# Kernel optimization log

Hardware: AMD Instinct MI355X
Metric: run time of the kernel (lower is better)

The kernel has to match this reference:

```python
import jax, jax.numpy as jnp
import numpy as np

N = 100000
E = 1600000
DIM = 64
HEADS = 8
HEAD_DIM = DIM // HEADS
LN_EPS = 1e-5
NORM_EPS = 1e-12


def setup_inputs() -> dict:
    key = jax.random.key(0)
    ks = jax.random.split(key, 5)
    x = jax.random.normal(ks[0], (N, DIM), dtype=jnp.float32)
    edge_index = jax.random.randint(ks[1], (2, E), 0, N, dtype=jnp.int32)
    W_w = jax.random.normal(ks[2], (DIM, DIM), dtype=jnp.float32) * (1.0 / np.sqrt(DIM))
    W_b = jax.random.normal(ks[3], (DIM,), dtype=jnp.float32) * 0.01
    a = jax.random.normal(ks[4], (HEADS, 2 * HEAD_DIM), dtype=jnp.float32) * 0.1
    ln_scale = jnp.ones((DIM,), dtype=jnp.float32)
    ln_bias = jnp.zeros((DIM,), dtype=jnp.float32)
    return {"x": x, "edge_index": edge_index, "W_w": W_w, "W_b": W_b,
            "a": a, "ln_scale": ln_scale, "ln_bias": ln_bias}


def reference(x, edge_index, W_w, W_b, a, ln_scale, ln_bias):
    n = x.shape[0]
    # Linear (dropout = identity in eval), reshape to heads
    h = (x @ W_w.T + W_b).reshape(n, HEADS, HEAD_DIM)          # [N,H,D]
    src, dst = edge_index[0], edge_index[1]
    hs = h[src]                                                 # [E,H,D]
    hd = h[dst]                                                 # [E,H,D]
    a_src, a_dst = a[:, :HEAD_DIM], a[:, HEAD_DIM:]             # [H,D] each
    # (a * cat(hs, hd)).sum(-1) split over the two halves
    alpha = jnp.einsum('ehd,hd->eh', hs, a_src) + jnp.einsum('ehd,hd->eh', hd, a_dst)
    alpha = jnp.where(alpha >= 0, alpha, 0.2 * alpha)           # LeakyReLU(0.2)
    alpha = jax.nn.softmax(alpha, axis=1)                       # NOTE: over heads, as in source
    msg = alpha[..., None] * hd                                 # [E,H,D]
    out = jax.ops.segment_sum(msg, src, num_segments=n)         # scatter-add to src nodes
    out = out.reshape(n, DIM)
    # residual + LayerNorm
    y = out + x
    mu = jnp.mean(y, axis=-1, keepdims=True)
    var = jnp.mean((y - mu) ** 2, axis=-1, keepdims=True)
    y = (y - mu) * jax.lax.rsqrt(var + LN_EPS) * ln_scale + ln_bias
    # F.normalize(p=2, dim=-1)
    norm = jnp.sqrt(jnp.sum(y * y, axis=-1, keepdims=True))
    return y / jnp.maximum(norm, NORM_EPS)
```

## Files before the change

### kernel.cpp

```cpp
#include <hip/hip_runtime.h>
#include <hip/hip_fp16.h>
#include <math.h>

#define N_NODES 100000
#define N_EDGES 1600000
#define LN_EPS 1e-5f
#define NORM_EPS 1e-12f
#define ROWS_PER_BLOCK 32
#define GEMM_BLOCKS (N_NODES / ROWS_PER_BLOCK)
#define WSTRIDE 66
#define REC_BYTES 32
#define WB 64
#define NBKT ((N_NODES + WB - 1) / WB)
#define BIN_TILE 8192
#define BIN_BLOCKS ((N_EDGES + BIN_TILE - 1) / BIN_TILE)

__global__ __launch_bounds__(256) void k_gemm(
    const float* __restrict__ x, const float* __restrict__ W,
    const float* __restrict__ b, const float* __restrict__ a,
    __half* __restrict__ h16,
    float* __restrict__ s_src, float* __restrict__ s_dst)
{
    __shared__ float WL[64 * WSTRIDE];
    __shared__ float xs[ROWS_PER_BLOCK * 64];
    const int tid  = threadIdx.x;
    const int lane = tid & 63;
    const int wv   = tid >> 6;

    for (int idx = tid * 4; idx < 64 * 64; idx += 256 * 4) {
        const float4 w = *(const float4*)(W + idx);
        const int c = idx >> 6, k = idx & 63;
        WL[c * WSTRIDE + k + 0] = w.x;
        WL[c * WSTRIDE + k + 1] = w.y;
        WL[c * WSTRIDE + k + 2] = w.z;
        WL[c * WSTRIDE + k + 3] = w.w;
    }
    const int row0 = blockIdx.x * ROWS_PER_BLOCK;
    for (int idx = tid * 4; idx < ROWS_PER_BLOCK * 64; idx += 256 * 4)
        *(float4*)(xs + idx) = *(const float4*)(x + (size_t)row0 * 64 + idx);
    __syncthreads();

    const float bias = b[lane];
    float acc[8];
    #pragma unroll
    for (int r = 0; r < 8; ++r) acc[r] = bias;

    const int rbase = wv * 8;
    const float* wrow = WL + lane * WSTRIDE;
    const float* xrow = xs + rbase * 64;
    #pragma unroll 1
    for (int kk = 0; kk < 64; kk += 4) {
        const float2 w01 = *(const float2*)(wrow + kk);
        const float2 w23 = *(const float2*)(wrow + kk + 2);
        #pragma unroll
        for (int r = 0; r < 8; ++r) {
            const float4 xq = *(const float4*)(xrow + r * 64 + kk);
            acc[r] += xq.x * w01.x + xq.y * w01.y + xq.z * w23.x + xq.w * w23.y;
        }
    }

    const float asrc = a[(lane >> 3) * 16 + (lane & 7)];
    const float adst = a[(lane >> 3) * 16 + 8 + (lane & 7)];
    #pragma unroll
    for (int r = 0; r < 8; ++r) {
        const int row = row0 + rbase + r;
        const float v = acc[r];
        h16[(size_t)row * 64 + lane] = __float2half_rn(v);
        float p = v * asrc, q = v * adst;
        p += __shfl_xor(p, 1);  q += __shfl_xor(q, 1);
        p += __shfl_xor(p, 2);  q += __shfl_xor(q, 2);
        p += __shfl_xor(p, 4);  q += __shfl_xor(q, 4);
        if ((lane & 7) == 0) {
            s_src[row * 8 + (lane >> 3)] = p;
            s_dst[row * 8 + (lane >> 3)] = q;
        }
    }
}

__global__ __launch_bounds__(1024) void k_hist(
    const int* __restrict__ ei, int* __restrict__ bhist)
{
    __shared__ int hist[NBKT];
    const int tid = threadIdx.x;
    for (int b = tid; b < NBKT; b += 1024) hist[b] = 0;
    __syncthreads();
    const int e0 = blockIdx.x * BIN_TILE;
    #pragma unroll
    for (int j = 0; j < 8; ++j) {
        const int e = e0 + j * 1024 + tid;
        if (e < N_EDGES) atomicAdd(&hist[ei[e] >> 6], 1);
    }
    __syncthreads();
    for (int b = tid; b < NBKT; b += 1024)
        if (hist[b]) atomicAdd(&bhist[b], hist[b]);
}

__global__ __launch_bounds__(1024) void k_bscan(
    const int* __restrict__ bhist, int* __restrict__ bucket_base,
    int* __restrict__ gbin)
{
    __shared__ int wsum[16];
    const int tid = threadIdx.x, lane = tid & 63, wv = tid >> 6;

    int v = (tid < NBKT) ? bhist[tid] : 0;
    int sc = v;
    #pragma unroll
    for (int off = 1; off < 64; off <<= 1) {
        int t = __shfl_up(sc, off);
        if (lane >= off) sc += t;
    }
    if (lane == 63) wsum[wv] = sc;
    __syncthreads();
    if (tid < 16) {
        int ws = wsum[tid];
        #pragma unroll
        for (int off = 1; off < 16; off <<= 1) {
            int t = __shfl_up(ws, off);
            if (tid >= off) ws += t;
        }
        wsum[tid] = ws;
    }
    __syncthreads();
    const int pref0 = wv ? wsum[wv - 1] : 0;
    const int ex0 = pref0 + sc - v;
    if (tid < NBKT) { bucket_base[tid] = ex0; gbin[tid] = ex0; }
    const int T1 = wsum[15];
    __syncthreads();

    const int i2 = 1024 + tid;
    int v2 = (i2 < NBKT) ? bhist[i2] : 0;
    int sc2 = v2;
    #pragma unroll
    for (int off = 1; off < 64; off <<= 1) {
        int t = __shfl_up(sc2, off);
        if (lane >= off) sc2 += t;
    }
    if (lane == 63) wsum[wv] = sc2;
    __syncthreads();
    if (tid < 16) {
        int ws = wsum[tid];
        #pragma unroll
        for (int off = 1; off < 16; off <<= 1) {
            int t = __shfl_up(ws, off);
            if (tid >= off) ws += t;
        }
        wsum[tid] = ws;
    }
    __syncthreads();
    const int pref1 = wv ? wsum[wv - 1] : 0;
    const int ex1 = T1 + pref1 + sc2 - v2;
    if (i2 < NBKT) { bucket_base[i2] = ex1; gbin[i2] = ex1; }
    if (tid == 0) bucket_base[NBKT] = N_EDGES;
}

__global__ __launch_bounds__(1024) void k_bin(
    const int* __restrict__ ei, int* __restrict__ gbin,
    int2* __restrict__ staged)
{
    __shared__ int hist[NBKT];
    __shared__ int base[NBKT];
    const int tid = threadIdx.x;
    for (int b = tid; b < NBKT; b += 1024) hist[b] = 0;
    __syncthreads();

    int s[8], d[8], r[8];
    const int e0 = blockIdx.x * BIN_TILE;
    #pragma unroll
    for (int j = 0; j < 8; ++j) {
        const int e = e0 + j * 1024 + tid;
        if (e < N_EDGES) {
            s[j] = ei[e];
            d[j] = ei[N_EDGES + e];
            r[j] = atomicAdd(&hist[s[j] >> 6], 1);
        }
    }
    __syncthreads();
    for (int b = tid; b < NBKT; b += 1024)
        if (hist[b]) base[b] = atomicAdd(&gbin[b], hist[b]);
    __syncthreads();
    #pragma unroll
    for (int j = 0; j < 8; ++j) {
        const int e = e0 + j * 1024 + tid;
        if (e < N_EDGES)
            staged[(size_t)base[s[j] >> 6] + r[j]] = make_int2(s[j], d[j]);
    }
}

__global__ __launch_bounds__(1024) void k_place(
    const int* __restrict__ bucket_base, const int2* __restrict__ staged,
    const float* __restrict__ s_src, const float* __restrict__ s_dst,
    int* __restrict__ row_ptr, char* __restrict__ rec)
{
    __shared__ int cnt[WB];
    __shared__ int cur[WB];
    const int g   = blockIdx.x;
    const int n0  = g * WB;
    const int tid = threadIdx.x;
    if (tid < WB) cnt[tid] = 0;
    __syncthreads();
    const int beg = bucket_base[g];
    const int end = bucket_base[g + 1];

    for (int j = beg + tid; j < end; j += 1024)
        atomicAdd(&cnt[staged[j].x - n0], 1);
    __syncthreads();
    if (tid < WB) {
        const int c = cnt[tid];
        int sc = c;
        #pragma unroll
        for (int off = 1; off < 64; off <<= 1) {
            int t = __shfl_up(sc, off);
            if (tid >= off) sc += t;
        }
        const int rp = beg + sc - c;
        cur[tid] = rp;
        if (n0 + tid < N_NODES) row_ptr[n0 + tid] = rp;
    }
    if (g == NBKT - 1 && tid == 0) row_ptr[N_NODES] = N_EDGES;
    __syncthreads();

    for (int j = beg + tid; j < end; j += 1024) {
        const int2 sd = staged[j];
        const int src = sd.x, dst = sd.y;

        const float4 a0 = *(const float4*)(s_src + (size_t)src * 8);
        const float4 a1 = *(const float4*)(s_src + (size_t)src * 8 + 4);
        const float4 b0 = *(const float4*)(s_dst + (size_t)dst * 8);
        const float4 b1 = *(const float4*)(s_dst + (size_t)dst * 8 + 4);
        float sc[8] = {a0.x + b0.x, a0.y + b0.y, a0.z + b0.z, a0.w + b0.w,
                       a1.x + b1.x, a1.y + b1.y, a1.z + b1.z, a1.w + b1.w};
        float m = -1e30f;
        #pragma unroll
        for (int h = 0; h < 8; ++h) {
            sc[h] = (sc[h] >= 0.f) ? sc[h] : 0.2f * sc[h];
            m = fmaxf(m, sc[h]);
        }
        float sum = 0.f;
        #pragma unroll
        for (int h = 0; h < 8; ++h) { sc[h] = __expf(sc[h] - m); sum += sc[h]; }
        const float inv = 1.f / sum;
        unsigned int q[4];
        #pragma unroll
        for (int jj = 0; jj < 4; ++jj) {
            const unsigned short lo = __half_as_ushort(__float2half_rn(sc[2*jj]   * inv));
            const unsigned short hi = __half_as_ushort(__float2half_rn(sc[2*jj+1] * inv));
            q[jj] = (unsigned int)lo | ((unsigned int)hi << 16);
        }

        const int slot = atomicAdd(&cur[src - n0], 1);
        char* rcd = rec + (size_t)slot * REC_BYTES;
        *(uint4*)rcd        = make_uint4(q[0], q[1], q[2], q[3]);
        *(uint4*)(rcd + 16) = make_uint4((unsigned)dst, 0u, 0u, 0u);
    }
}

__global__ __launch_bounds__(256) void k_gather(
    const int* __restrict__ row_ptr, const char* __restrict__ rec,
    const __half* __restrict__ h16,
    const float* __restrict__ x, const float* __restrict__ ln_scale,
    const float* __restrict__ ln_bias, float* __restrict__ out)
{
    const int i = blockIdx.x * 4 + (threadIdx.x >> 6);
    if (i >= N_NODES) return;
    const int lane = threadIdx.x & 63;
    const int head = lane >> 3;

    const int beg = row_ptr[i];
    const int end = row_ptr[i + 1];
    const float xres = x[(size_t)i * 64 + lane];

    float acc = 0.f;
    int e = beg;
    for (; e + 3 < end; e += 4) {
        const char* r0 = rec + (size_t)(e + 0) * REC_BYTES;
        const char* r1 = rec + (size_t)(e + 1) * REC_BYTES;
        const char* r2 = rec + (size_t)(e + 2) * REC_BYTES;
        const char* r3 = rec + (size_t)(e + 3) * REC_BYTES;
        const int d0 = *(const int*)(r0 + 16);
        const int d1 = *(const int*)(r1 + 16);
        const int d2 = *(const int*)(r2 + 16);
        const int d3 = *(const int*)(r3 + 16);
        const float al0 = __half2float(*(const __half*)(r0 + (head << 1)));
        const float al1 = __half2float(*(const __half*)(r1 + (head << 1)));
        const float al2 = __half2float(*(const __half*)(r2 + (head << 1)));
        const float al3 = __half2float(*(const __half*)(r3 + (head << 1)));
        const float h0 = __half2float(h16[(size_t)d0 * 64 + lane]);
        const float h1 = __half2float(h16[(size_t)d1 * 64 + lane]);
        const float h2 = __half2float(h16[(size_t)d2 * 64 + lane]);
        const float h3 = __half2float(h16[(size_t)d3 * 64 + lane]);
        acc += al0 * h0 + al1 * h1 + al2 * h2 + al3 * h3;
    }
    for (; e < end; ++e) {
        const char* r = rec + (size_t)e * REC_BYTES;
        acc += __half2float(*(const __half*)(r + (head << 1))) *
               __half2float(h16[(size_t)(*(const int*)(r + 16)) * 64 + lane]);
    }

    float v = acc + xres;
    float s = v;
    #pragma unroll
    for (int off = 1; off < 64; off <<= 1) s += __shfl_xor(s, off);
    const float mu = s * (1.f / 64.f);
    const float d = v - mu;
    float vs = d * d;
    #pragma unroll
    for (int off = 1; off < 64; off <<= 1) vs += __shfl_xor(vs, off);
    const float var = vs * (1.f / 64.f);
    float y = d * rsqrtf(var + LN_EPS) * ln_scale[lane] + ln_bias[lane];
    float ss = y * y;
    #pragma unroll
    for (int off = 1; off < 64; off <<= 1) ss += __shfl_xor(ss, off);
    const float norm = sqrtf(ss);
    out[(size_t)i * 64 + lane] = y / fmaxf(norm, NORM_EPS);
}

extern "C" void kernel_launch(void* const* d_in, const int* in_sizes, int n_in,
                              void* d_out, int out_size, void* d_ws, size_t ws_size,
                              hipStream_t stream)
{
    const float* x        = (const float*)d_in[0];
    const int*   ei       = (const int*)d_in[1];
    const float* W        = (const float*)d_in[2];
    const float* b        = (const float*)d_in[3];
    const float* a        = (const float*)d_in[4];
    const float* ln_scale = (const float*)d_in[5];
    const float* ln_bias  = (const float*)d_in[6];
    float* out = (float*)d_out;

    char* ws = (char*)d_ws;
    size_t off = 0;
    auto alloc = [&](size_t bytes) {
        void* p = ws + off;
        off = (off + bytes + 255) & ~(size_t)255;
        return p;
    };
    __half* h16       = (__half*)alloc((size_t)N_NODES * 64 * 2);
    float* s_src      = (float*) alloc((size_t)N_NODES * 8 * 4);
    float* s_dst      = (float*) alloc((size_t)N_NODES * 8 * 4);
    int*   bhist      = (int*)   alloc((size_t)NBKT * 4);
    int*   bucket_base= (int*)   alloc((size_t)(NBKT + 1) * 4);
    int*   gbin       = (int*)   alloc((size_t)NBKT * 4);
    int*   row_ptr    = (int*)   alloc((size_t)(N_NODES + 1) * 4);
    int2*  staged     = (int2*)  alloc((size_t)N_EDGES * 8);
    char*  rec        = (char*)  alloc((size_t)N_EDGES * REC_BYTES);

    hipMemsetAsync(bhist, 0, (size_t)NBKT * 4, stream);

    k_hist  <<<BIN_BLOCKS, 1024, 0, stream>>>(ei, bhist);
    k_bscan <<<1, 1024, 0, stream>>>(bhist, bucket_base, gbin);
    k_gemm  <<<GEMM_BLOCKS, 256, 0, stream>>>(x, W, b, a, h16, s_src, s_dst);
    k_bin   <<<BIN_BLOCKS, 1024, 0, stream>>>(ei, gbin, staged);
    k_place <<<NBKT, 1024, 0, stream>>>(bucket_base, staged, s_src, s_dst,
                                        row_ptr, rec);
    k_gather<<<(N_NODES + 3) / 4, 256, 0, stream>>>(row_ptr, rec,
                                                    h16, x,
                                                    ln_scale, ln_bias, out);
}
```

Before: 254.1 us.

## Fuse edge placement and gather into per-bucket shared-memory scatter-add with LayerNorm

Removes the per-node CSR build (row_ptr, 32-byte edge records) and the separate gather kernel. Each 64-node bucket block now computes attention weights for chunks of its edges into LDS, then scatter-adds alpha*h[dst] into a 64x64 shared accumulator with LDS atomics, and finishes with residual, LayerNorm and L2 normalize in the same kernel. Staged edges are packed into one 32-bit word (local src in 6 bits, dst in the rest), halving staging traffic. The trade-offs are LDS atomic contention, serialized per-wave loops over 64 edges each, and only ~1563 blocks of 1024 threads for the whole gather.

```diff
diff --git a/kernel.cpp b/kernel.cpp
--- a/kernel.cpp
+++ b/kernel.cpp
@@ -9,11 +9,11 @@
 #define ROWS_PER_BLOCK 32
 #define GEMM_BLOCKS (N_NODES / ROWS_PER_BLOCK)
 #define WSTRIDE 66
-#define REC_BYTES 32
 #define WB 64
 #define NBKT ((N_NODES + WB - 1) / WB)
 #define BIN_TILE 8192
 #define BIN_BLOCKS ((N_EDGES + BIN_TILE - 1) / BIN_TILE)
+#define QCHUNK 1024
 
 __global__ __launch_bounds__(256) void k_gemm(
     const float* __restrict__ x, const float* __restrict__ W,
@@ -155,7 +155,7 @@
 
 __global__ __launch_bounds__(1024) void k_bin(
     const int* __restrict__ ei, int* __restrict__ gbin,
-    int2* __restrict__ staged)
+    unsigned int* __restrict__ staged)
 {
     __shared__ int hist[NBKT];
     __shared__ int base[NBKT];
@@ -182,136 +182,102 @@
     for (int j = 0; j < 8; ++j) {
         const int e = e0 + j * 1024 + tid;
         if (e < N_EDGES)
-            staged[(size_t)base[s[j] >> 6] + r[j]] = make_int2(s[j], d[j]);
+            staged[(size_t)base[s[j] >> 6] + r[j]] =
+                (unsigned int)((s[j] & 63) | (d[j] << 6));
     }
 }
 
 __global__ __launch_bounds__(1024) void k_place(
-    const int* __restrict__ bucket_base, const int2* __restrict__ staged,
+    const int* __restrict__ bucket_base, const unsigned int* __restrict__ staged,
     const float* __restrict__ s_src, const float* __restrict__ s_dst,
-    int* __restrict__ row_ptr, char* __restrict__ rec)
-{
-    __shared__ int cnt[WB];
-    __shared__ int cur[WB];
-    const int g   = blockIdx.x;
-    const int n0  = g * WB;
-    const int tid = threadIdx.x;
-    if (tid < WB) cnt[tid] = 0;
-    __syncthreads();
+    const __half* __restrict__ h16, const float* __restrict__ x,
+    const float* __restrict__ ln_scale, const float* __restrict__ ln_bias,
+    float* __restrict__ out)
+{
+    __shared__ float accs[WB * 64];
+    __shared__ uint4 qa[QCHUNK];
+    __shared__ unsigned int qm[QCHUNK];
+    const int g    = blockIdx.x;
+    const int n0   = g * WB;
+    const int tid  = threadIdx.x;
+    const int lane = tid & 63;
+    const int wv   = tid >> 6;
+
+    #pragma unroll
+    for (int k = tid; k < WB * 64; k += 1024) accs[k] = 0.f;
     const int beg = bucket_base[g];
     const int end = bucket_base[g + 1];
-
-    for (int j = beg + tid; j < end; j += 1024)
-        atomicAdd(&cnt[staged[j].x - n0], 1);
-    __syncthreads();
-    if (tid < WB) {
-        const int c = cnt[tid];
-        int sc = c;
-        #pragma unroll
-        for (int off = 1; off < 64; off <<= 1) {
-            int t = __shfl_up(sc, off);
-            if (tid >= off) sc += t;
-        }
-        const int rp = beg + sc - c;
-        cur[tid] = rp;
-        if (n0 + tid < N_NODES) row_ptr[n0 + tid] = rp;
-    }
-    if (g == NBKT - 1 && tid == 0) row_ptr[N_NODES] = N_EDGES;
-    __syncthreads();
-
-    for (int j = beg + tid; j < end; j += 1024) {
-        const int2 sd = staged[j];
-        const int src = sd.x, dst = sd.y;
-
-        const float4 a0 = *(const float4*)(s_src + (size_t)src * 8);
-        const float4 a1 = *(const float4*)(s_src + (size_t)src * 8 + 4);
-        const float4 b0 = *(const float4*)(s_dst + (size_t)dst * 8);
-        const float4 b1 = *(const float4*)(s_dst + (size_t)dst * 8 + 4);
-        float sc[8] = {a0.x + b0.x, a0.y + b0.y, a0.z + b0.z, a0.w + b0.w,
-                       a1.x + b1.x, a1.y + b1.y, a1.z + b1.z, a1.w + b1.w};
-        float m = -1e30f;
-        #pragma unroll
-        for (int h = 0; h < 8; ++h) {
-            sc[h] = (sc[h] >= 0.f) ? sc[h] : 0.2f * sc[h];
-            m = fmaxf(m, sc[h]);
-        }
-        float sum = 0.f;
-        #pragma unroll
-        for (int h = 0; h < 8; ++h) { sc[h] = __expf(sc[h] - m); sum += sc[h]; }
-        const float inv = 1.f / sum;
-        unsigned int q[4];
-        #pragma unroll
-        for (int jj = 0; jj < 4; ++jj) {
-            const unsigned short lo = __half_as_ushort(__float2half_rn(sc[2*jj]   * inv));
-            const unsigned short hi = __half_as_ushort(__float2half_rn(sc[2*jj+1] * inv));
-            q[jj] = (unsigned int)lo | ((unsigned int)hi << 16);
-        }
-
-        const int slot = atomicAdd(&cur[src - n0], 1);
-        char* rcd = rec + (size_t)slot * REC_BYTES;
-        *(uint4*)rcd        = make_uint4(q[0], q[1], q[2], q[3]);
-        *(uint4*)(rcd + 16) = make_uint4((unsigned)dst, 0u, 0u, 0u);
-    }
-}
-
-__global__ __launch_bounds__(256) void k_gather(
-    const int* __restrict__ row_ptr, const char* __restrict__ rec,
-    const __half* __restrict__ h16,
-    const float* __restrict__ x, const float* __restrict__ ln_scale,
-    const float* __restrict__ ln_bias, float* __restrict__ out)
-{
-    const int i = blockIdx.x * 4 + (threadIdx.x >> 6);
-    if (i >= N_NODES) return;
-    const int lane = threadIdx.x & 63;
-    const int head = lane >> 3;
-
-    const int beg = row_ptr[i];
-    const int end = row_ptr[i + 1];
-    const float xres = x[(size_t)i * 64 + lane];
-
-    float acc = 0.f;
-    int e = beg;
-    for (; e + 3 < end; e += 4) {
-        const char* r0 = rec + (size_t)(e + 0) * REC_BYTES;
-        const char* r1 = rec + (size_t)(e + 1) * REC_BYTES;
-        const char* r2 = rec + (size_t)(e + 2) * REC_BYTES;
-        const char* r3 = rec + (size_t)(e + 3) * REC_BYTES;
-        const int d0 = *(const int*)(r0 + 16);
-        const int d1 = *(const int*)(r1 + 16);
-        const int d2 = *(const int*)(r2 + 16);
-        const int d3 = *(const int*)(r3 + 16);
-        const float al0 = __half2float(*(const __half*)(r0 + (head << 1)));
-        const float al1 = __half2float(*(const __half*)(r1 + (head << 1)));
-        const float al2 = __half2float(*(const __half*)(r2 + (head << 1)));
-        const float al3 = __half2float(*(const __half*)(r3 + (head << 1)));
-        const float h0 = __half2float(h16[(size_t)d0 * 64 + lane]);
-        const float h1 = __half2float(h16[(size_t)d1 * 64 + lane]);
-        const float h2 = __half2float(h16[(size_t)d2 * 64 + lane]);
-        const float h3 = __half2float(h16[(size_t)d3 * 64 + lane]);
-        acc += al0 * h0 + al1 * h1 + al2 * h2 + al3 * h3;
-    }
-    for (; e < end; ++e) {
-        const char* r = rec + (size_t)e * REC_BYTES;
-        acc += __half2float(*(const __half*)(r + (head << 1))) *
-               __half2float(h16[(size_t)(*(const int*)(r + 16)) * 64 + lane]);
-    }
-
-    float v = acc + xres;
-    float s = v;
-    #pragma unroll
-    for (int off = 1; off < 64; off <<= 1) s += __shfl_xor(s, off);
-    const float mu = s * (1.f / 64.f);
-    const float d = v - mu;
-    float vs = d * d;
-    #pragma unroll
-    for (int off = 1; off < 64; off <<= 1) vs += __shfl_xor(vs, off);
-    const float var = vs * (1.f / 64.f);
-    float y = d * rsqrtf(var + LN_EPS) * ln_scale[lane] + ln_bias[lane];
-    float ss = y * y;
-    #pragma unroll
-    for (int off = 1; off < 64; off <<= 1) ss += __shfl_xor(ss, off);
-    const float norm = sqrtf(ss);
-    out[(size_t)i * 64 + lane] = y / fmaxf(norm, NORM_EPS);
+    __syncthreads();
+
+    for (int cb = beg; cb < end; cb += QCHUNK) {
+        const int m = min(QCHUNK, end - cb);
+        if (tid < m) {
+            const unsigned int w = staged[cb + tid];
+            const int src = n0 + (int)(w & 63u);
+            const int dst = (int)(w >> 6);
+
+            const float4 a0 = *(const float4*)(s_src + (size_t)src * 8);
+            const float4 a1 = *(const float4*)(s_src + (size_t)src * 8 + 4);
+            const float4 b0 = *(const float4*)(s_dst + (size_t)dst * 8);
+            const float4 b1 = *(const float4*)(s_dst + (size_t)dst * 8 + 4);
+            float sc[8] = {a0.x + b0.x, a0.y + b0.y, a0.z + b0.z, a0.w + b0.w,
+                           a1.x + b1.x, a1.y + b1.y, a1.z + b1.z, a1.w + b1.w};
+            float mx = -1e30f;
+            #pragma unroll
+            for (int h = 0; h < 8; ++h) {
+                sc[h] = (sc[h] >= 0.f) ? sc[h] : 0.2f * sc[h];
+                mx = fmaxf(mx, sc[h]);
+            }
+            float sum = 0.f;
+            #pragma unroll
+            for (int h = 0; h < 8; ++h) { sc[h] = __expf(sc[h] - mx); sum += sc[h]; }
+            const float inv = 1.f / sum;
+            unsigned int q[4];
+            #pragma unroll
+            for (int jj = 0; jj < 4; ++jj) {
+                const unsigned short lo = __half_as_ushort(__float2half_rn(sc[2*jj]   * inv));
+                const unsigned short hi = __half_as_ushort(__float2half_rn(sc[2*jj+1] * inv));
+                q[jj] = (unsigned int)lo | ((unsigned int)hi << 16);
+            }
+            qa[tid] = make_uint4(q[0], q[1], q[2], q[3]);
+            qm[tid] = w;
+        }
+        __syncthreads();
+
+        const int k0 = wv * 64;
+        const int kcnt = min(64, m - k0);
+        for (int k = 0; k < kcnt; ++k) {
+            const unsigned int w = qm[k0 + k];
+            const float al = __half2float(
+                ((const __half*)(qa + k0 + k))[lane >> 3]);
+            const float hv = __half2float(h16[(size_t)(w >> 6) * 64 + lane]);
+            atomicAdd(&accs[(w & 63u) * 64 + lane], al * hv);
+        }
+        __syncthreads();
+    }
+
+    #pragma unroll 1
+    for (int r = 0; r < 4; ++r) {
+        const int nl = wv * 4 + r;
+        const int i  = n0 + nl;
+        if (i >= N_NODES) continue;
+        float v = accs[nl * 64 + lane] + x[(size_t)i * 64 + lane];
+        float s = v;
+        #pragma unroll
+        for (int off = 1; off < 64; off <<= 1) s += __shfl_xor(s, off);
+        const float mu = s * (1.f / 64.f);
+        const float d = v - mu;
+        float vs = d * d;
+        #pragma unroll
+        for (int off = 1; off < 64; off <<= 1) vs += __shfl_xor(vs, off);
+        const float var = vs * (1.f / 64.f);
+        float y = d * rsqrtf(var + LN_EPS) * ln_scale[lane] + ln_bias[lane];
+        float ss = y * y;
+        #pragma unroll
+        for (int off = 1; off < 64; off <<= 1) ss += __shfl_xor(ss, off);
+        const float norm = sqrtf(ss);
+        out[(size_t)i * 64 + lane] = y / fmaxf(norm, NORM_EPS);
+    }
 }
 
 extern "C" void kernel_launch(void* const* d_in, const int* in_sizes, int n_in,
@@ -334,15 +300,13 @@
         off = (off + bytes + 255) & ~(size_t)255;
         return p;
     };
-    __half* h16       = (__half*)alloc((size_t)N_NODES * 64 * 2);
-    float* s_src      = (float*) alloc((size_t)N_NODES * 8 * 4);
-    float* s_dst      = (float*) alloc((size_t)N_NODES * 8 * 4);
-    int*   bhist      = (int*)   alloc((size_t)NBKT * 4);
-    int*   bucket_base= (int*)   alloc((size_t)(NBKT + 1) * 4);
-    int*   gbin       = (int*)   alloc((size_t)NBKT * 4);
-    int*   row_ptr    = (int*)   alloc((size_t)(N_NODES + 1) * 4);
-    int2*  staged     = (int2*)  alloc((size_t)N_EDGES * 8);
-    char*  rec        = (char*)  alloc((size_t)N_EDGES * REC_BYTES);
+    __half* h16        = (__half*)alloc((size_t)N_NODES * 64 * 2);
+    float*  s_src      = (float*) alloc((size_t)N_NODES * 8 * 4);
+    float*  s_dst      = (float*) alloc((size_t)N_NODES * 8 * 4);
+    int*    bhist      = (int*)   alloc((size_t)NBKT * 4);
+    int*    bucket_base= (int*)   alloc((size_t)(NBKT + 1) * 4);
+    int*    gbin       = (int*)   alloc((size_t)NBKT * 4);
+    unsigned int* staged = (unsigned int*)alloc((size_t)N_EDGES * 4);
 
     hipMemsetAsync(bhist, 0, (size_t)NBKT * 4, stream);
 
@@ -351,8 +315,5 @@
     k_gemm  <<<GEMM_BLOCKS, 256, 0, stream>>>(x, W, b, a, h16, s_src, s_dst);
     k_bin   <<<BIN_BLOCKS, 1024, 0, stream>>>(ei, gbin, staged);
     k_place <<<NBKT, 1024, 0, stream>>>(bucket_base, staged, s_src, s_dst,
-                                        row_ptr, rec);
-    k_gather<<<(N_NODES + 3) / 4, 256, 0, stream>>>(row_ptr, rec,
-                                                    h16, x,
-                                                    ln_scale, ln_bias, out);
-}
+                                        h16, x, ln_scale, ln_bias, out);
+}
```

After: 783.0 us. 3.08x slower.

## Pack staged edges into 32-bit words and split records into SoA arrays

Applied to the files above, without the earlier changes.

Edges staged between binning and placement are packed as a 6-bit local source index plus the destination index in one 32-bit word, halving that traffic. The 32-byte padded per-edge record is replaced by separate dst_sorted (4 B) and alpha16 (16 B) arrays, removing wasted padding bytes in writes and reads. The gather loop is unrolled to 8 edges to put more independent loads in flight. Packing relies on dst fitting in 26 bits, which holds for N=100000.

```diff
diff --git a/kernel.cpp b/kernel.cpp
--- a/kernel.cpp
+++ b/kernel.cpp
@@ -9,7 +9,6 @@
 #define ROWS_PER_BLOCK 32
 #define GEMM_BLOCKS (N_NODES / ROWS_PER_BLOCK)
 #define WSTRIDE 66
-#define REC_BYTES 32
 #define WB 64
 #define NBKT ((N_NODES + WB - 1) / WB)
 #define BIN_TILE 8192
@@ -155,7 +154,7 @@
 
 __global__ __launch_bounds__(1024) void k_bin(
     const int* __restrict__ ei, int* __restrict__ gbin,
-    int2* __restrict__ staged)
+    unsigned int* __restrict__ staged)
 {
     __shared__ int hist[NBKT];
     __shared__ int base[NBKT];
@@ -182,14 +181,16 @@
     for (int j = 0; j < 8; ++j) {
         const int e = e0 + j * 1024 + tid;
         if (e < N_EDGES)
-            staged[(size_t)base[s[j] >> 6] + r[j]] = make_int2(s[j], d[j]);
+            staged[(size_t)base[s[j] >> 6] + r[j]] =
+                (unsigned int)((s[j] & 63) | (d[j] << 6));
     }
 }
 
 __global__ __launch_bounds__(1024) void k_place(
-    const int* __restrict__ bucket_base, const int2* __restrict__ staged,
+    const int* __restrict__ bucket_base, const unsigned int* __restrict__ staged,
     const float* __restrict__ s_src, const float* __restrict__ s_dst,
-    int* __restrict__ row_ptr, char* __restrict__ rec)
+    int* __restrict__ row_ptr, int* __restrict__ dst_sorted,
+    __half* __restrict__ alpha16)
 {
     __shared__ int cnt[WB];
     __shared__ int cur[WB];
@@ -202,7 +203,7 @@
     const int end = bucket_base[g + 1];
 
     for (int j = beg + tid; j < end; j += 1024)
-        atomicAdd(&cnt[staged[j].x - n0], 1);
+        atomicAdd(&cnt[staged[j] & 63u], 1);
     __syncthreads();
     if (tid < WB) {
         const int c = cnt[tid];
@@ -220,11 +221,12 @@
     __syncthreads();
 
     for (int j = beg + tid; j < end; j += 1024) {
-        const int2 sd = staged[j];
-        const int src = sd.x, dst = sd.y;
-
-        const float4 a0 = *(const float4*)(s_src + (size_t)src * 8);
-        const float4 a1 = *(const float4*)(s_src + (size_t)src * 8 + 4);
+        const unsigned int w = staged[j];
+        const int srcl = (int)(w & 63u);
+        const int dst  = (int)(w >> 6);
+
+        const float4 a0 = *(const float4*)(s_src + (size_t)(n0 + srcl) * 8);
+        const float4 a1 = *(const float4*)(s_src + (size_t)(n0 + srcl) * 8 + 4);
         const float4 b0 = *(const float4*)(s_dst + (size_t)dst * 8);
         const float4 b1 = *(const float4*)(s_dst + (size_t)dst * 8 + 4);
         float sc[8] = {a0.x + b0.x, a0.y + b0.y, a0.z + b0.z, a0.w + b0.w,
@@ -247,16 +249,15 @@
             q[jj] = (unsigned int)lo | ((unsigned int)hi << 16);
         }
 
-        const int slot = atomicAdd(&cur[src - n0], 1);
-        char* rcd = rec + (size_t)slot * REC_BYTES;
-        *(uint4*)rcd        = make_uint4(q[0], q[1], q[2], q[3]);
-        *(uint4*)(rcd + 16) = make_uint4((unsigned)dst, 0u, 0u, 0u);
+        const int slot = atomicAdd(&cur[srcl], 1);
+        dst_sorted[slot] = dst;
+        *(uint4*)(alpha16 + (size_t)slot * 8) = make_uint4(q[0], q[1], q[2], q[3]);
     }
 }
 
 __global__ __launch_bounds__(256) void k_gather(
-    const int* __restrict__ row_ptr, const char* __restrict__ rec,
-    const __half* __restrict__ h16,
+    const int* __restrict__ row_ptr, const int* __restrict__ dst_sorted,
+    const __half* __restrict__ alpha16, const __half* __restrict__ h16,
     const float* __restrict__ x, const float* __restrict__ ln_scale,
     const float* __restrict__ ln_bias, float* __restrict__ out)
 {
@@ -269,32 +270,40 @@
     const int end = row_ptr[i + 1];
     const float xres = x[(size_t)i * 64 + lane];
 
+    const __half* __restrict__ hp = h16 + lane;
+    const __half* __restrict__ ap = alpha16 + head;
+
     float acc = 0.f;
     int e = beg;
+    for (; e + 7 < end; e += 8) {
+        int d[8];
+        #pragma unroll
+        for (int j = 0; j < 8; ++j) d[j] = dst_sorted[e + j];
+        float al[8];
+        #pragma unroll
+        for (int j = 0; j < 8; ++j) al[j] = __half2float(ap[(e + j) * 8]);
+        float hv[8];
+        #pragma unroll
+        for (int j = 0; j < 8; ++j) hv[j] = __half2float(hp[d[j] * 64]);
+        #pragma unroll
+        for (int j = 0; j < 8; ++j) acc = fmaf(al[j], hv[j], acc);
+    }
     for (; e + 3 < end; e += 4) {
-        const char* r0 = rec + (size_t)(e + 0) * REC_BYTES;
-        const char* r1 = rec + (size_t)(e + 1) * REC_BYTES;
-        const char* r2 = rec + (size_t)(e + 2) * REC_BYTES;
-        const char* r3 = rec + (size_t)(e + 3) * REC_BYTES;
-        const int d0 = *(const int*)(r0 + 16);
-        const int d1 = *(const int*)(r1 + 16);
-        const int d2 = *(const int*)(r2 + 16);
-        const int d3 = *(const int*)(r3 + 16);
-        const float al0 = __half2float(*(const __half*)(r0 + (head << 1)));
-        const float al1 = __half2float(*(const __half*)(r1 + (head << 1)));
-        const float al2 = __half2float(*(const __half*)(r2 + (head << 1)));
-        const float al3 = __half2float(*(const __half*)(r3 + (head << 1)));
-        const float h0 = __half2float(h16[(size_t)d0 * 64 + lane]);
-        const float h1 = __half2float(h16[(size_t)d1 * 64 + lane]);
-        const float h2 = __half2float(h16[(size_t)d2 * 64 + lane]);
-        const float h3 = __half2float(h16[(size_t)d3 * 64 + lane]);
-        acc += al0 * h0 + al1 * h1 + al2 * h2 + al3 * h3;
-    }
-    for (; e < end; ++e) {
-        const char* r = rec + (size_t)e * REC_BYTES;
-        acc += __half2float(*(const __half*)(r + (head << 1))) *
-               __half2float(h16[(size_t)(*(const int*)(r + 16)) * 64 + lane]);
-    }
+        int d[4];
+        #pragma unroll
+        for (int j = 0; j < 4; ++j) d[j] = dst_sorted[e + j];
+        float al[4];
+        #pragma unroll
+        for (int j = 0; j < 4; ++j) al[j] = __half2float(ap[(e + j) * 8]);
+        float hv[4];
+        #pragma unroll
+        for (int j = 0; j < 4; ++j) hv[j] = __half2float(hp[d[j] * 64]);
+        #pragma unroll
+        for (int j = 0; j < 4; ++j) acc = fmaf(al[j], hv[j], acc);
+    }
+    for (; e < end; ++e)
+        acc = fmaf(__half2float(ap[e * 8]),
+                   __half2float(hp[dst_sorted[e] * 64]), acc);
 
     float v = acc + xres;
     float s = v;
@@ -334,15 +343,16 @@
         off = (off + bytes + 255) & ~(size_t)255;
         return p;
     };
-    __half* h16       = (__half*)alloc((size_t)N_NODES * 64 * 2);
-    float* s_src      = (float*) alloc((size_t)N_NODES * 8 * 4);
-    float* s_dst      = (float*) alloc((size_t)N_NODES * 8 * 4);
-    int*   bhist      = (int*)   alloc((size_t)NBKT * 4);
-    int*   bucket_base= (int*)   alloc((size_t)(NBKT + 1) * 4);
-    int*   gbin       = (int*)   alloc((size_t)NBKT * 4);
-    int*   row_ptr    = (int*)   alloc((size_t)(N_NODES + 1) * 4);
-    int2*  staged     = (int2*)  alloc((size_t)N_EDGES * 8);
-    char*  rec        = (char*)  alloc((size_t)N_EDGES * REC_BYTES);
+    __half* h16        = (__half*)alloc((size_t)N_NODES * 64 * 2);
+    float*  s_src      = (float*) alloc((size_t)N_NODES * 8 * 4);
+    float*  s_dst      = (float*) alloc((size_t)N_NODES * 8 * 4);
+    int*    bhist      = (int*)   alloc((size_t)NBKT * 4);
+    int*    bucket_base= (int*)   alloc((size_t)(NBKT + 1) * 4);
+    int*    gbin       = (int*)   alloc((size_t)NBKT * 4);
+    int*    row_ptr    = (int*)   alloc((size_t)(N_NODES + 1) * 4);
+    unsigned int* staged = (unsigned int*)alloc((size_t)N_EDGES * 4);
+    int*    dst_sorted = (int*)   alloc((size_t)N_EDGES * 4);
+    __half* alpha16    = (__half*)alloc((size_t)N_EDGES * 8 * 2);
 
     hipMemsetAsync(bhist, 0, (size_t)NBKT * 4, stream);
 
@@ -351,8 +361,7 @@
     k_gemm  <<<GEMM_BLOCKS, 256, 0, stream>>>(x, W, b, a, h16, s_src, s_dst);
     k_bin   <<<BIN_BLOCKS, 1024, 0, stream>>>(ei, gbin, staged);
     k_place <<<NBKT, 1024, 0, stream>>>(bucket_base, staged, s_src, s_dst,
-                                        row_ptr, rec);
-    k_gather<<<(N_NODES + 3) / 4, 256, 0, stream>>>(row_ptr, rec,
-                                                    h16, x,
-                                                    ln_scale, ln_bias, out);
-}
+                                        row_ptr, dst_sorted, alpha16);
+    k_gather<<<(N_NODES + 3) / 4, 256, 0, stream>>>(row_ptr, dst_sorted, alpha16,
+                                                    h16, x, ln_scale, ln_bias, out);
+}
```

Result: faster. 234.7 us (-7.6%).
